# Kernel tuning notes

Measured on AMD Instinct MI355X. Metric: run time of the kernel, lower is better.

## Reference

```python
import jax, jax.numpy as jnp
import numpy as np
import math

B = 128        # batch (= bipartite matching N)
L = 16         # detector layers (MAX_LAYER)
E = 768        # n_embd
D = E // 2     # RFF target_dim
H = 12         # n_head
HD = E // H    # head_size
NL = 6         # n_layer
SEQ = 12       # tokens after concats: 3+3 -> 6 -> +currentLayer -> 12
MAX_LAYER = L
LN_EPS = 1e-3  # keras LayerNormalization default


def setup_inputs() -> dict:
    key = jax.random.key(0)
    ks = jax.random.split(key, 8)
    inp = {}
    inp["X"] = jax.random.normal(ks[0], (B, L, 3), dtype=jnp.float32) * 50.0
    inp["targets"] = jax.random.normal(ks[1], (B, L, 3), dtype=jnp.float32)
    # RandomFourierFeatures params (random per-call in original; fixed here):
    # x: xmin=-160,xmax=160,n=9*1024 ; y: n=12*512 ; dE: xmin=0,xmax=230,n=2300
    specs = [(-160.0, 160.0, 9 * 1024), (-160.0, 160.0, 12 * 512), (0.0, 230.0, 2300)]
    om, ph = [], []
    for i, (xmin, xmax, n) in enumerate(specs):
        k1, k2 = jax.random.split(jax.random.fold_in(ks[2], i))
        omin = 2.0 * math.pi / (xmax - xmin)
        lo, hi = math.log(omin / n), math.log(omin)
        om.append(jnp.exp(jax.random.uniform(k1, (D,), minval=lo, maxval=hi)))
        ph.append(jax.random.uniform(k2, (D,)))  # B ~ U(0,1)*scale, scale=1
    inp["omegas"] = jnp.stack(om).astype(jnp.float32)  # (3, D)
    inp["phases"] = jnp.stack(ph).astype(jnp.float32)  # (3, D)
    # np.random.permutation per layer-step, fixed here
    inp["perms"] = jnp.stack(
        [jax.random.permutation(jax.random.fold_in(ks[3], i), B) for i in range(L - 1)]
    ).astype(jnp.int32)  # (L-1, B)
    # transformer weights (stacked over layers)
    kk = jax.random.split(ks[4], 16)
    s = 0.02
    inp["Wq"] = jax.random.normal(kk[0], (NL, E, H, HD)) * s
    inp["bq"] = jnp.zeros((NL, H, HD))
    inp["Wk"] = jax.random.normal(kk[1], (NL, E, H, HD)) * s
    inp["bk"] = jnp.zeros((NL, H, HD))
    inp["Wv"] = jax.random.normal(kk[2], (NL, E, H, HD)) * s
    inp["bv"] = jnp.zeros((NL, H, HD))
    inp["Wo"] = jax.random.normal(kk[3], (NL, H, HD, E)) * s
    inp["bo"] = jnp.zeros((NL, E))
    inp["ln1g"] = jnp.ones((NL, E)); inp["ln1b"] = jnp.zeros((NL, E))
    inp["ln2g"] = jnp.ones((NL, E)); inp["ln2b"] = jnp.zeros((NL, E))
    inp["W1"] = jax.random.normal(kk[4], (NL, E, 4 * E)) * s
    inp["b1f"] = jnp.zeros((NL, 4 * E))
    inp["W2"] = jax.random.normal(kk[5], (NL, 4 * E, E)) * s
    inp["b2f"] = jnp.zeros((NL, E))
    inp["lnfg"] = jnp.ones((E,)); inp["lnfb"] = jnp.zeros((E,))
    inp["Wout"] = jax.random.normal(kk[6], (SEQ * E, 3)) * s
    inp["bout"] = jnp.zeros((3,))
    return inp


def _ln(x, g, b):
    mu = jnp.mean(x, -1, keepdims=True)
    v = jnp.var(x, -1, keepdims=True)
    return (x - mu) * jax.lax.rsqrt(v + LN_EPS) * g + b


def _greedy_match(cost):
    """Greedy bipartite matching: sort all NxN costs ascending, assign first-come.
    Returns row_to_col_match_vec (N,) int32."""
    N = cost.shape[0]
    order = jnp.argsort(cost.reshape(-1))

    def step(carry, k):
        row, col = carry
        i = k // N
        j = k % N
        ok = (row[i] == -1) & (col[j] == -1)
        row = row.at[i].set(jnp.where(ok, j, row[i]))
        col = col.at[j].set(jnp.where(ok, i, col[j]))
        return (row, col), None

    init = (jnp.full((N,), -1, jnp.int32), jnp.full((N,), -1, jnp.int32))
    (row, _), _ = jax.lax.scan(step, init, order)
    return row


def _forward(X, targets, omegas, phases, perms, Wq, bq, Wk, bk, Wv, bv, Wo, bo,
             ln1g, ln1b, ln2g, ln2b, W1, b1f, W2, b2f, lnfg, lnfb, Wout, bout):
    # RFF: (B,L,3) -> (B,L,3,D)
    XS = jnp.cos(X[..., None] * omegas[None, None, :, :] + phases[None, None, :, :])
    losses = []
    scale = 1.0 / math.sqrt(HD)
    for lidx in range(1, L):
        xc = XS[:, -lidx]        # (B,3,D)
        xp = XS[:, -lidx - 1]    # (B,3,D)
        x = jnp.concatenate([xc, xp], axis=2)            # (B,3,E)
        y = targets[:, -lidx + 1]                        # (B,3)
        y_prev = jnp.broadcast_to(y[:, :, None], (B, 3, E))
        x = jnp.concatenate([x, y_prev], axis=1)         # (B,6,E)
        cur = jnp.full_like(x, float(MAX_LAYER - lidx))
        x = jnp.concatenate([x, cur], axis=1)            # (B,12,E)
        x = x[perms[lidx - 1]]                           # batch permutation
        for l in range(NL):
            h = _ln(x, ln1g[l], ln1b[l])
            q = jnp.einsum('bse,ehd->bshd', h, Wq[l]) + bq[l]
            k = jnp.einsum('bse,ehd->bshd', h, Wk[l]) + bk[l]
            v = jnp.einsum('bse,ehd->bshd', h, Wv[l]) + bv[l]
            att = jax.nn.softmax(jnp.einsum('bqhd,bkhd->bhqk', q, k) * scale, axis=-1)
            o = jnp.einsum('bhqk,bkhd->bqhd', att, v)
            x = x + (jnp.einsum('bqhd,hde->bqe', o, Wo[l]) + bo[l])
            h = _ln(x, ln2g[l], ln2b[l])
            x = x + (jnp.maximum(h @ W1[l] + b1f[l], 0.0) @ W2[l] + b2f[l])
        x = _ln(x, lnfg, lnfb).reshape(B, SEQ * E)
        logits = x @ Wout + bout                         # (B,3)
        tgt = targets[:, -lidx]                          # (B,3)
        cost = jnp.sqrt(jnp.sum((logits[:, None, :] - tgt[None, :, :]) ** 2, axis=-1) + 1e-12)
        m = _greedy_match(jax.lax.stop_gradient(cost))
        lm = logits[m]                                   # gather per original
        losses.append(jnp.mean((lm - tgt) ** 2))
    return jnp.mean(jnp.stack(losses))


def reference(X, targets, omegas, phases, perms, Wq, bq, Wk, bk, Wv, bv, Wo, bo,
              ln1g, ln1b, ln2g, ln2b, W1, b1f, W2, b2f, lnfg, lnfb, Wout, bout):
    return _forward(X, targets, omegas, phases, perms, Wq, bq, Wk, bk, Wv, bv, Wo, bo,
                    ln1g, ln1b, ln2g, ln2b, W1, b1f, W2, b2f, lnfg, lnfb, Wout, bout)
```

## Files before the change

kernel.cpp:

```cpp
#include <hip/hip_runtime.h>
#include <hip/hip_bf16.h>
#include <math.h>

#define B_   128
#define L_   16
#define E_   768
#define D_   384
#define H_   12
#define HD_  64
#define NL_  6
#define SEQ_ 12
#define LN_EPS 0.001f
#define WLS   7077888
#define BQS   2304

typedef __attribute__((ext_vector_type(8))) short bf16x8;
typedef __attribute__((ext_vector_type(4))) float f32x4;
typedef unsigned long long u64;

#define GLOAD_LDS16(g, l) \
    __builtin_amdgcn_global_load_lds((__attribute__((address_space(1))) const void*)(g), \
                                     (__attribute__((address_space(3))) void*)(l), 16, 0, 0)

__global__ __launch_bounds__(256) void k_x0(const float* __restrict__ X,
                                            const float* __restrict__ targets,
                                            const int* __restrict__ perms,
                                            const float* __restrict__ om,
                                            const float* __restrict__ ph,
                                            float* __restrict__ x, int cb, int ntok) {
    int i = blockIdx.x * 256 + threadIdx.x;
    if (i >= ntok*E_) return;
    int e   = i % E_;
    int tok = i / E_;
    int s   = tok % SEQ_;
    int bi  = (tok / SEQ_) % B_;
    int c   = tok / (SEQ_*B_);
    int cl  = cb + c;
    int lidx = cl + 1;
    int pb  = perms[cl*B_ + bi];
    float val;
    if (s < 3) {
        int t  = (e < D_) ? (L_ - lidx) : (L_ - lidx - 1);
        int dd = (e < D_) ? e : (e - D_);
        float xv = X[(pb*L_ + t)*3 + s];
        val = cosf(xv * om[s*D_ + dd] + ph[s*D_ + dd]);
    } else if (s < 6) {
        int t = (17 - lidx) & 15;
        val = targets[(pb*L_ + t)*3 + (s - 3)];
    } else {
        val = (float)(L_ - lidx);
    }
    x[i] = val;
}

__global__ __launch_bounds__(256) void k_ln(const float* __restrict__ x,
                                            const float* __restrict__ g,
                                            const float* __restrict__ b,
                                            __hip_bfloat16* __restrict__ h) {
    int gi = blockIdx.x * 256 + threadIdx.x;
    int tok = gi >> 6, lane = gi & 63;
    const float4* xr = (const float4*)(x + (size_t)tok * E_);
    float4 v0 = xr[lane], v1 = xr[lane + 64], v2 = xr[lane + 128];
    float s = v0.x+v0.y+v0.z+v0.w + v1.x+v1.y+v1.z+v1.w + v2.x+v2.y+v2.z+v2.w;
    #pragma unroll
    for (int o = 32; o > 0; o >>= 1) s += __shfl_xor(s, o, 64);
    float mu = s * (1.0f / E_);
    v0.x-=mu; v0.y-=mu; v0.z-=mu; v0.w-=mu;
    v1.x-=mu; v1.y-=mu; v1.z-=mu; v1.w-=mu;
    v2.x-=mu; v2.y-=mu; v2.z-=mu; v2.w-=mu;
    float q = v0.x*v0.x+v0.y*v0.y+v0.z*v0.z+v0.w*v0.w
            + v1.x*v1.x+v1.y*v1.y+v1.z*v1.z+v1.w*v1.w
            + v2.x*v2.x+v2.y*v2.y+v2.z*v2.z+v2.w*v2.w;
    #pragma unroll
    for (int o = 32; o > 0; o >>= 1) q += __shfl_xor(q, o, 64);
    float rstd = rsqrtf(q * (1.0f / E_) + LN_EPS);
    const float4* g4 = (const float4*)g;
    const float4* b4 = (const float4*)b;
    ushort4* h4 = (ushort4*)(h + (size_t)tok * E_);
    #pragma unroll
    for (int k = 0; k < 3; k++) {
        float4 v = (k == 0) ? v0 : (k == 1) ? v1 : v2;
        float4 gg = g4[lane + k*64], bb = b4[lane + k*64];
        ushort4 o;
        o.x = __bfloat16_as_ushort(__float2bfloat16(v.x * rstd * gg.x + bb.x));
        o.y = __bfloat16_as_ushort(__float2bfloat16(v.y * rstd * gg.y + bb.y));
        o.z = __bfloat16_as_ushort(__float2bfloat16(v.z * rstd * gg.z + bb.z));
        o.w = __bfloat16_as_ushort(__float2bfloat16(v.w * rstd * gg.w + bb.w));
        h4[lane + k*64] = o;
    }
}

__global__ __launch_bounds__(256) void k_cvt(const float* __restrict__ Wq,
                                             const float* __restrict__ Wk,
                                             const float* __restrict__ Wv,
                                             const float* __restrict__ Wo,
                                             const float* __restrict__ W1,
                                             const float* __restrict__ W2,
                                             const float* __restrict__ bq,
                                             const float* __restrict__ bk,
                                             const float* __restrict__ bv,
                                             __hip_bfloat16* __restrict__ wl0,
                                             float* __restrict__ bqkv0, int lbase) {
    int bid = blockIdx.x;
    int l   = lbase + bid / 6913;
    bid %= 6913;
    __hip_bfloat16* wl = wl0 + (size_t)(l - lbase) * WLS;
    float* bqkv = bqkv0 + (l - lbase) * BQS;
    int tid = threadIdx.x;
    if (bid == 6912) {
        for (int i = tid; i < 2304; i += 256) {
            float v = (i < 768) ? bq[l*768 + i] : (i < 1536) ? bk[l*768 + i - 768]
                                                             : bv[l*768 + i - 1536];
            bqkv[i] = v;
        }
        return;
    }
    const float* src; __hip_bfloat16* dst; int K, N, ti, tj;
    if (bid < 1728) {
        int part = bid / 576, idx = bid % 576;
        const float* srcs[3] = {Wq, Wk, Wv};
        src = srcs[part] + (size_t)l*768*768; dst = wl + (size_t)part*768*768;
        K = 768; N = 768; tj = idx % 24; ti = idx / 24;
    } else if (bid < 2304) {
        int idx = bid - 1728;
        src = Wo + (size_t)l*768*768; dst = wl + 1769472;
        K = 768; N = 768; tj = idx % 24; ti = idx / 24;
    } else if (bid < 4608) {
        int idx = bid - 2304;
        src = W1 + (size_t)l*768*3072; dst = wl + 2359296;
        K = 768; N = 3072; tj = idx % 96; ti = idx / 96;
    } else {
        int idx = bid - 4608;
        src = W2 + (size_t)l*3072*768; dst = wl + 4718592;
        K = 3072; N = 768; tj = idx % 24; ti = idx / 24;
    }
    __shared__ float tbuf[32][33];
    int tx = tid & 31, ty = tid >> 5;
    #pragma unroll
    for (int p = 0; p < 4; p++) {
        int k = ti*32 + ty + p*8, n = tj*32 + tx;
        tbuf[ty + p*8][tx] = src[(size_t)k*N + n];
    }
    __syncthreads();
    #pragma unroll
    for (int p = 0; p < 4; p++) {
        int n = tj*32 + ty + p*8, k = ti*32 + tx;
        dst[(size_t)n*K + k] = __float2bfloat16(tbuf[tx][ty + p*8]);
    }
}

template<int BN_>
__global__ __launch_bounds__(256) void k_gemm_t(const __hip_bfloat16* __restrict__ A,
                                                const __hip_bfloat16* __restrict__ Bt,
                                                const float* __restrict__ bias,
                                                void* __restrict__ Cp,
                                                int K, int ldb, int ldc, int flags) {
    constexpr int NF = BN_ / 32;
    __shared__ __align__(16) char smem[8192 + BN_*64];
    char* As = smem;
    char* Bs = smem + 8192;
    int tid = threadIdx.x;
    int lane = tid & 63;
    int w = tid >> 6;
    int wm = (w >> 1) * 64, wn = (w & 1) * (BN_/2);
    int m0 = blockIdx.y * 128, n0 = blockIdx.x * BN_;

    int u1 = tid, u2 = tid + 256;
    int r1 = u1 >> 2, kg1 = ((u1 & 3) ^ ((r1 >> 1) & 3)) * 8;
    int r2 = u2 >> 2, kg2 = ((u2 & 3) ^ ((r2 >> 1) & 3)) * 8;

    f32x4 acc[4][NF] = {};
    int fr = lane & 15, fkg = lane >> 4;

    for (int k0 = 0; k0 < K; k0 += 32) {
        GLOAD_LDS16(A  + (size_t)(m0 + r1) * K   + k0 + kg1, As + u1 * 16);
        GLOAD_LDS16(A  + (size_t)(m0 + r2) * K   + k0 + kg2, As + u2 * 16);
        GLOAD_LDS16(Bt + (size_t)(n0 + r1) * ldb + k0 + kg1, Bs + u1 * 16);
        if (BN_ == 128)
            GLOAD_LDS16(Bt + (size_t)(n0 + r2) * ldb + k0 + kg2, Bs + u2 * 16);
        __syncthreads();
        bf16x8 a[4], b[NF];
        #pragma unroll
        for (int i = 0; i < 4; i++) {
            int m = wm + i*16 + fr;
            a[i] = *(const bf16x8*)(As + m*64 + ((fkg ^ ((m >> 1) & 3)) * 16));
        }
        #pragma unroll
        for (int j = 0; j < NF; j++) {
            int n = wn + j*16 + fr;
            b[j] = *(const bf16x8*)(Bs + n*64 + ((fkg ^ ((n >> 1) & 3)) * 16));
        }
        #pragma unroll
        for (int i = 0; i < 4; i++)
            #pragma unroll
            for (int j = 0; j < NF; j++)
                acc[i][j] = __builtin_amdgcn_mfma_f32_16x16x32_bf16(a[i], b[j], acc[i][j], 0, 0, 0);
        __syncthreads();
    }

    int colL = lane & 15, rowg = (lane >> 4) * 4;
    #pragma unroll
    for (int i = 0; i < 4; i++) {
        #pragma unroll
        for (int j = 0; j < NF; j++) {
            int col = n0 + wn + j*16 + colL;
            float bv = bias ? bias[col] : 0.0f;
            #pragma unroll
            for (int r = 0; r < 4; r++) {
                int row = m0 + wm + i*16 + rowg + r;
                float v = acc[i][j][r] + bv;
                if (flags & 4) v = fmaxf(v, 0.0f);
                size_t off = (size_t)row * ldc + col;
                if (flags & 1)      ((__hip_bfloat16*)Cp)[off] = __float2bfloat16(v);
                else if (flags & 2) ((float*)Cp)[off] += v;
                else                ((float*)Cp)[off] = v;
            }
        }
    }
}

__global__ __launch_bounds__(256) void k_attn(const __hip_bfloat16* __restrict__ qkv,
                                              __hip_bfloat16* __restrict__ o) {
    __shared__ float qs[SEQ_][HD_], ks[SEQ_][HD_], vs[SEQ_][HD_];
    __shared__ float att[SEQ_][SEQ_];
    int blk = blockIdx.x;
    int hh  = blk % H_;
    int cbb = blk / H_;
    int t = threadIdx.x;
    if (t < 96) {
        int s = t >> 3, c = (t & 7) * 8;
        size_t base = (size_t)(cbb*SEQ_ + s) * 2304 + hh*64 + c;
        bf16x8 q8 = *(const bf16x8*)(qkv + base);
        bf16x8 k8 = *(const bf16x8*)(qkv + base + 768);
        bf16x8 v8 = *(const bf16x8*)(qkv + base + 1536);
        #pragma unroll
        for (int j = 0; j < 8; j++) {
            qs[s][c+j] = __uint_as_float((unsigned)(unsigned short)q8[j] << 16);
            ks[s][c+j] = __uint_as_float((unsigned)(unsigned short)k8[j] << 16);
            vs[s][c+j] = __uint_as_float((unsigned)(unsigned short)v8[j] << 16);
        }
    }
    __syncthreads();
    if (t < SEQ_*SEQ_) {
        int qi = t / SEQ_, kj = t % SEQ_;
        float s = 0.f;
        #pragma unroll
        for (int d = 0; d < HD_; d++) s += qs[qi][d] * ks[kj][d];
        att[qi][kj] = s * 0.125f;
    }
    __syncthreads();
    if (t < SEQ_) {
        float mx = -1e30f;
        #pragma unroll
        for (int j = 0; j < SEQ_; j++) mx = fmaxf(mx, att[t][j]);
        float e[SEQ_]; float sum = 0.f;
        #pragma unroll
        for (int j = 0; j < SEQ_; j++) { e[j] = expf(att[t][j] - mx); sum += e[j]; }
        float inv = 1.f / sum;
        #pragma unroll
        for (int j = 0; j < SEQ_; j++) att[t][j] = e[j] * inv;
    }
    __syncthreads();
    for (int i = t; i < SEQ_*HD_; i += 256) {
        int s = i / HD_, d = i % HD_;
        float acc = 0.f;
        #pragma unroll
        for (int j = 0; j < SEQ_; j++) acc += att[s][j] * vs[j][d];
        o[(size_t)(cbb*SEQ_ + s) * 768 + hh*64 + d] = __float2bfloat16(acc);
    }
}

__global__ __launch_bounds__(256) void k_logits(const __hip_bfloat16* __restrict__ hfin,
                                                const float* __restrict__ Wout,
                                                const float* __restrict__ bout,
                                                float* __restrict__ logits, int cb) {
    __shared__ float red[3][256];
    int blk = blockIdx.x;
    int t = threadIdx.x;
    const __hip_bfloat16* row = hfin + (size_t)blk * SEQ_ * E_;
    float a0 = 0.f, a1 = 0.f, a2 = 0.f;
    for (int e = t; e < SEQ_*E_; e += 256) {
        float x = __bfloat162float(row[e]);
        a0 += x * Wout[e*3 + 0]; a1 += x * Wout[e*3 + 1]; a2 += x * Wout[e*3 + 2];
    }
    red[0][t] = a0; red[1][t] = a1; red[2][t] = a2;
    __syncthreads();
    for (int o = 128; o > 0; o >>= 1) {
        if (t < o) { red[0][t] += red[0][t+o]; red[1][t] += red[1][t+o]; red[2][t] += red[2][t+o]; }
        __syncthreads();
    }
    if (t < 3) logits[((size_t)cb*B_ + blk)*3 + t] = red[t][0] + bout[t];
}

__global__ __launch_bounds__(64) void k_match(const float* __restrict__ logits,
                                              const float* __restrict__ targets,
                                              float* __restrict__ losses) {
    __shared__ float cst[128 * 129];
    __shared__ float tg[128][3];
    __shared__ int mrow[128];
    int cl = blockIdx.x, lane = threadIdx.x;
    int lidx = cl + 1;
    for (int j = lane; j < 128; j += 64) {
        const float* tp = &targets[((size_t)j*L_ + (L_ - lidx)) * 3];
        tg[j][0] = tp[0]; tg[j][1] = tp[1]; tg[j][2] = tp[2];
    }
    __syncthreads();
    u64 kc[2];
    #pragma unroll
    for (int hh = 0; hh < 2; hh++) {
        int r = lane + hh*64;
        const float* lg = &logits[(cl*B_ + r) * 3];
        float l0 = lg[0], l1 = lg[1], l2 = lg[2];
        u64 best = ~0ull;
        for (int c = 0; c < 128; c++) {
            float d0 = l0 - tg[c][0], d1 = l1 - tg[c][1], d2 = l2 - tg[c][2];
            float cc = sqrtf(d0*d0 + d1*d1 + d2*d2 + 1e-12f);
            cst[r*129 + c] = cc;
            u64 key = ((u64)__float_as_uint(cc) << 14) | (unsigned)(r*128 + c);
            best = key < best ? key : best;
        }
        kc[hh] = best;
    }
    __syncthreads();
    u64 dead0 = 0, dead1 = 0;
    int done = 0;
    for (int trip = 0; trip < 16640 && done < 128; trip++) {
        u64 b = kc[0] < kc[1] ? kc[0] : kc[1];
        #pragma unroll
        for (int o = 32; o > 0; o >>= 1) {
            u64 x = __shfl_xor(b, o, 64);
            b = x < b ? x : b;
        }
        unsigned e  = (unsigned)b & 0x3fffu;
        unsigned wi = e >> 7, wj = e & 127;
        bool isDead = (((wj < 64) ? (dead0 >> wj) : (dead1 >> (wj - 64))) & 1ull) != 0;
        if (!isDead) {
            if ((wi & 63u) == (unsigned)lane) {
                mrow[wi] = (int)wj;
                kc[wi >> 6] = ~0ull;
            }
            if (wj < 64) dead0 |= 1ull << wj; else dead1 |= 1ull << (wj - 64);
            done++;
        } else {
            float c0 = cst[wi*129 + lane];
            float c1 = cst[wi*129 + lane + 64];
            bool d0b = ((dead0 >> lane) & 1ull) != 0;
            bool d1b = ((dead1 >> lane) & 1ull) != 0;
            u64 k0 = d0b ? ~0ull : (((u64)__float_as_uint(c0) << 14) | (unsigned)(wi*128 + lane));
            u64 k1 = d1b ? ~0ull : (((u64)__float_as_uint(c1) << 14) | (unsigned)(wi*128 + lane + 64));
            u64 nb = k0 < k1 ? k0 : k1;
            #pragma unroll
            for (int o = 32; o > 0; o >>= 1) {
                u64 x = __shfl_xor(nb, o, 64);
                nb = x < nb ? x : nb;
            }
            if ((wi & 63u) == (unsigned)lane) kc[wi >> 6] = nb;
        }
    }
    __syncthreads();
    float a = 0.f;
    #pragma unroll
    for (int hh = 0; hh < 2; hh++) {
        int r = lane + hh*64;
        const float* lg = &logits[(cl*B_ + mrow[r]) * 3];
        float d0 = lg[0]-tg[r][0], d1 = lg[1]-tg[r][1], d2 = lg[2]-tg[r][2];
        a += d0*d0 + d1*d1 + d2*d2;
    }
    #pragma unroll
    for (int o = 32; o > 0; o >>= 1) a += __shfl_xor(a, o, 64);
    if (lane == 0) losses[cl] = a * (1.0f / (B_*3));
}

__global__ void k_final(const float* __restrict__ losses, float* __restrict__ out) {
    float s = 0.f;
    for (int i = 0; i < 15; i++) s += losses[i];
    out[0] = s * (1.0f / 15.0f);
}

extern "C" void kernel_launch(void* const* d_in, const int* in_sizes, int n_in,
                              void* d_out, int out_size, void* d_ws, size_t ws_size,
                              hipStream_t stream) {
    (void)in_sizes; (void)n_in; (void)out_size;
    const float* X       = (const float*)d_in[0];
    const float* targets = (const float*)d_in[1];
    const float* omegas  = (const float*)d_in[2];
    const float* phases  = (const float*)d_in[3];
    const int*   perms   = (const int*)d_in[4];
    const float* Wq  = (const float*)d_in[5];
    const float* bq  = (const float*)d_in[6];
    const float* Wk  = (const float*)d_in[7];
    const float* bk  = (const float*)d_in[8];
    const float* Wv  = (const float*)d_in[9];
    const float* bv  = (const float*)d_in[10];
    const float* Wo  = (const float*)d_in[11];
    const float* bo  = (const float*)d_in[12];
    const float* ln1g = (const float*)d_in[13];
    const float* ln1b = (const float*)d_in[14];
    const float* ln2g = (const float*)d_in[15];
    const float* ln2b = (const float*)d_in[16];
    const float* W1  = (const float*)d_in[17];
    const float* b1f = (const float*)d_in[18];
    const float* W2  = (const float*)d_in[19];
    const float* b2f = (const float*)d_in[20];
    const float* lnfg = (const float*)d_in[21];
    const float* lnfb = (const float*)d_in[22];
    const float* Wout = (const float*)d_in[23];
    const float* bout = (const float*)d_in[24];

    int CL; bool hoist;
    if (ws_size >= 263000000ull)      { CL = 15; hoist = false; }
    else if (ws_size >= 169000000ull) { CL = 5;  hoist = true;  }
    else                              { CL = 5;  hoist = false; }
    int M = CL * B_ * SEQ_;
    bool perLayerCvt = (CL == 15) || !hoist;

    char* wsb = (char*)d_ws;
    size_t off = 0;
    auto alloc = [&](size_t bytes) {
        char* p = wsb + off;
        off += (bytes + 255) & ~(size_t)255;
        return p;
    };
    float*          x      = (float*)alloc((size_t)M*E_*4);
    __hip_bfloat16* h      = (__hip_bfloat16*)alloc((size_t)M*E_*2);
    __hip_bfloat16* qkvh   = (__hip_bfloat16*)alloc((size_t)M*3072*2);
    __hip_bfloat16* wl     = (__hip_bfloat16*)alloc((hoist ? 6 : 1) * (size_t)WLS*2);
    float*          bqkv   = (float*)alloc((hoist ? 6 : 1) * (size_t)BQS*4);
    float*          logits = (float*)alloc(23040);
    float*          losses = (float*)alloc(64);

    if (hoist)
        k_cvt<<<6*6913, 256, 0, stream>>>(Wq, Wk, Wv, Wo, W1, W2, bq, bk, bv, wl, bqkv, 0);

    dim3 gQKV(2304/128, M/128);
    dim3 gF1 (3072/128, M/128);
    dim3 gN64(768/64,   M/128);
    dim3 gLN (M/4);

    for (int cb = 0; cb < 15; cb += CL) {
        k_x0<<<(M*E_)/256, 256, 0, stream>>>(X, targets, perms, omegas, phases, x, cb, M);
        for (int l = 0; l < NL_; l++) {
            __hip_bfloat16* wlp = hoist ? wl + (size_t)l*WLS : wl;
            float*          bqp = hoist ? bqkv + l*BQS : bqkv;
            if (perLayerCvt)
                k_cvt<<<6913, 256, 0, stream>>>(Wq, Wk, Wv, Wo, W1, W2, bq, bk, bv, wlp, bqp, l);
            k_ln<<<gLN, 256, 0, stream>>>(x, ln1g + l*E_, ln1b + l*E_, h);
            k_gemm_t<128><<<gQKV, 256, 0, stream>>>(h, wlp, bqp, qkvh, 768, 768, 2304, 1);
            k_attn<<<CL*B_*H_, 256, 0, stream>>>(qkvh, h);
            k_gemm_t<64><<<gN64, 256, 0, stream>>>(h, wlp + 1769472, bo + l*E_, x,
                                                   768, 768, 768, 2);
            k_ln<<<gLN, 256, 0, stream>>>(x, ln2g + l*E_, ln2b + l*E_, h);
            k_gemm_t<128><<<gF1, 256, 0, stream>>>(h, wlp + 2359296, b1f + l*3072, qkvh,
                                                   768, 768, 3072, 1|4);
            k_gemm_t<64><<<gN64, 256, 0, stream>>>(qkvh, wlp + 4718592, b2f + l*E_, x,
                                                   3072, 3072, 768, 2);
        }
        k_ln<<<gLN, 256, 0, stream>>>(x, lnfg, lnfb, h);
        k_logits<<<CL*B_, 256, 0, stream>>>(h, Wout, bout, logits, cb);
    }
    k_match<<<15, 64, 0, stream>>>(logits, targets, losses);
    k_final<<<1, 1, 0, stream>>>(losses, (float*)d_out);
}
```

Before: 5.075 ms.

## Replace GEMM with 256x256 double-buffered, 8-wave pipelined MFMA kernel

Replaces the 128xBN single-buffered GEMM with a 256x256-tile kernel of 512 threads that uses 128KB of LDS with double buffering and BK=64. Prefetching of the next k-tile is interleaved with MFMA phases, using explicit barriers and s_setprio. The aim is to raise arithmetic intensity and hide global-load latency. In exchange, it launches far fewer blocks (e.g. 3 column blocks for N=768), which can leave CUs idle when M is small. The very large LDS footprint also limits occupancy.

```diff
diff --git a/kernel.cpp b/kernel.cpp
--- a/kernel.cpp
+++ b/kernel.cpp
@@ -149,65 +149,142 @@
     }
 }
 
-template<int BN_>
-__global__ __launch_bounds__(256) void k_gemm_t(const __hip_bfloat16* __restrict__ A,
-                                                const __hip_bfloat16* __restrict__ Bt,
-                                                const float* __restrict__ bias,
-                                                void* __restrict__ Cp,
-                                                int K, int ldb, int ldc, int flags) {
-    constexpr int NF = BN_ / 32;
-    __shared__ __align__(16) char smem[8192 + BN_*64];
-    char* As = smem;
-    char* Bs = smem + 8192;
-    int tid = threadIdx.x;
-    int lane = tid & 63;
-    int w = tid >> 6;
-    int wm = (w >> 1) * 64, wn = (w & 1) * (BN_/2);
-    int m0 = blockIdx.y * 128, n0 = blockIdx.x * BN_;
-
-    int u1 = tid, u2 = tid + 256;
-    int r1 = u1 >> 2, kg1 = ((u1 & 3) ^ ((r1 >> 1) & 3)) * 8;
-    int r2 = u2 >> 2, kg2 = ((u2 & 3) ^ ((r2 >> 1) & 3)) * 8;
-
-    f32x4 acc[4][NF] = {};
-    int fr = lane & 15, fkg = lane >> 4;
-
-    for (int k0 = 0; k0 < K; k0 += 32) {
-        GLOAD_LDS16(A  + (size_t)(m0 + r1) * K   + k0 + kg1, As + u1 * 16);
-        GLOAD_LDS16(A  + (size_t)(m0 + r2) * K   + k0 + kg2, As + u2 * 16);
-        GLOAD_LDS16(Bt + (size_t)(n0 + r1) * ldb + k0 + kg1, Bs + u1 * 16);
-        if (BN_ == 128)
-            GLOAD_LDS16(Bt + (size_t)(n0 + r2) * ldb + k0 + kg2, Bs + u2 * 16);
-        __syncthreads();
-        bf16x8 a[4], b[NF];
-        #pragma unroll
-        for (int i = 0; i < 4; i++) {
-            int m = wm + i*16 + fr;
-            a[i] = *(const bf16x8*)(As + m*64 + ((fkg ^ ((m >> 1) & 3)) * 16));
-        }
-        #pragma unroll
-        for (int j = 0; j < NF; j++) {
-            int n = wn + j*16 + fr;
-            b[j] = *(const bf16x8*)(Bs + n*64 + ((fkg ^ ((n >> 1) & 3)) * 16));
-        }
+#define MFMA_BF16(a, b, c) __builtin_amdgcn_mfma_f32_16x16x32_bf16(a, b, c, 0, 0, 0)
+
+__global__ __launch_bounds__(512) void k_gemm256(const __hip_bfloat16* __restrict__ A,
+                                                 const __hip_bfloat16* __restrict__ Bt,
+                                                 const float* __restrict__ bias,
+                                                 void* __restrict__ Cp,
+                                                 int K, int ldb, int ldc, int flags) {
+    __shared__ __align__(16) char smem[131072];
+    const int tid  = threadIdx.x;
+    const int lane = tid & 63;
+    const int wid  = tid >> 6;
+    const int wr   = wid >> 2;
+    const int wc   = wid & 3;
+    const int m0   = blockIdx.y * 256;
+    const int n0   = blockIdx.x * 256;
+    const int fr   = lane & 15, fkg = lane >> 4, sx = fr & 7;
+    const int NT   = K >> 6;
+
+    const int srow = tid >> 3;
+    const int skc  = 8 * ((tid & 7) ^ ((tid >> 3) & 7));
+
+    const int aoff0 = (wr*128 + fr)*128 + (((0*4 + fkg) ^ sx) << 4);
+    const int aoff1 = (wr*128 + fr)*128 + (((1*4 + fkg) ^ sx) << 4);
+    const int boff0 = 32768 + (wc*64 + fr)*128 + (((0*4 + fkg) ^ sx) << 4);
+    const int boff1 = 32768 + (wc*64 + fr)*128 + (((1*4 + fkg) ^ sx) << 4);
+
+    f32x4 acc[8][4] = {};
+
+    auto stage = [&](int kt, int buf, int h) {
+        const __hip_bfloat16* mat = (h & 2) ? Bt : A;
+        const int ld   = (h & 2) ? ldb : K;
+        const int row0 = ((h & 2) ? n0 : m0) + (h & 1)*128;
+        char* d = smem + buf*65536 + ((h & 2) ? 32768 : 0) + (h & 1)*16384;
+        const int kk = kt*64 + skc;
+        GLOAD_LDS16(mat + (size_t)(row0 + srow)      * ld + kk, d + tid*16);
+        GLOAD_LDS16(mat + (size_t)(row0 + 64 + srow) * ld + kk, d + 8192 + tid*16);
+    };
+    auto ldA = [&](int buf, int i, int ks) -> bf16x8 {
+        return *(const bf16x8*)(smem + buf*65536 + i*2048 + (ks ? aoff1 : aoff0));
+    };
+    auto ldB = [&](int buf, int j, int ks) -> bf16x8 {
+        return *(const bf16x8*)(smem + buf*65536 + j*2048 + (ks ? boff1 : boff0));
+    };
+
+    stage(0, 0, 0); stage(0, 0, 1); stage(0, 0, 2); stage(0, 0, 3);
+    asm volatile("s_waitcnt vmcnt(0)" ::: "memory");
+    __syncthreads();
+
+    bf16x8 a[4][2], blo[2][2], bhi[2][2];
+
+    for (int kt = 0; kt < NT; ++kt) {
+        const int cur = kt & 1, nxt = cur ^ 1;
+        const bool pf = (kt + 1 < NT);
+
+        #pragma unroll
+        for (int i = 0; i < 4; i++) { a[i][0] = ldA(cur, i, 0); a[i][1] = ldA(cur, i, 1); }
+        #pragma unroll
+        for (int j = 0; j < 2; j++) { blo[j][0] = ldB(cur, j, 0); blo[j][1] = ldB(cur, j, 1); }
+        if (pf) { stage(kt+1, nxt, 0); stage(kt+1, nxt, 1); }
+        __builtin_amdgcn_sched_barrier(0);
+        __builtin_amdgcn_s_barrier();
+        asm volatile("s_waitcnt lgkmcnt(0)" ::: "memory");
+        __builtin_amdgcn_sched_barrier(0);
+        __builtin_amdgcn_s_setprio(1);
         #pragma unroll
         for (int i = 0; i < 4; i++)
             #pragma unroll
-            for (int j = 0; j < NF; j++)
-                acc[i][j] = __builtin_amdgcn_mfma_f32_16x16x32_bf16(a[i], b[j], acc[i][j], 0, 0, 0);
+            for (int j = 0; j < 2; j++) {
+                acc[i][j] = MFMA_BF16(a[i][0], blo[j][0], acc[i][j]);
+                acc[i][j] = MFMA_BF16(a[i][1], blo[j][1], acc[i][j]);
+            }
+        __builtin_amdgcn_s_setprio(0);
+        __builtin_amdgcn_sched_barrier(0);
+        __builtin_amdgcn_s_barrier();
+
+        #pragma unroll
+        for (int j = 0; j < 2; j++) { bhi[j][0] = ldB(cur, j+2, 0); bhi[j][1] = ldB(cur, j+2, 1); }
+        if (pf) { stage(kt+1, nxt, 2); stage(kt+1, nxt, 3); }
+        __builtin_amdgcn_sched_barrier(0);
+        __builtin_amdgcn_s_barrier();
+        asm volatile("s_waitcnt lgkmcnt(0)" ::: "memory");
+        __builtin_amdgcn_sched_barrier(0);
+        __builtin_amdgcn_s_setprio(1);
+        #pragma unroll
+        for (int i = 0; i < 4; i++)
+            #pragma unroll
+            for (int j = 0; j < 2; j++) {
+                acc[i][j+2] = MFMA_BF16(a[i][0], bhi[j][0], acc[i][j+2]);
+                acc[i][j+2] = MFMA_BF16(a[i][1], bhi[j][1], acc[i][j+2]);
+            }
+        __builtin_amdgcn_s_setprio(0);
+        __builtin_amdgcn_sched_barrier(0);
+        __builtin_amdgcn_s_barrier();
+
+        #pragma unroll
+        for (int i = 0; i < 4; i++) { a[i][0] = ldA(cur, i+4, 0); a[i][1] = ldA(cur, i+4, 1); }
+        __builtin_amdgcn_sched_barrier(0);
+        __builtin_amdgcn_s_barrier();
+        asm volatile("s_waitcnt lgkmcnt(0)" ::: "memory");
+        __builtin_amdgcn_sched_barrier(0);
+        __builtin_amdgcn_s_setprio(1);
+        #pragma unroll
+        for (int i = 0; i < 4; i++)
+            #pragma unroll
+            for (int j = 0; j < 2; j++) {
+                acc[i+4][j+2] = MFMA_BF16(a[i][0], bhi[j][0], acc[i+4][j+2]);
+                acc[i+4][j+2] = MFMA_BF16(a[i][1], bhi[j][1], acc[i+4][j+2]);
+            }
+        __builtin_amdgcn_s_setprio(0);
+        __builtin_amdgcn_sched_barrier(0);
+        __builtin_amdgcn_s_barrier();
+
+        __builtin_amdgcn_s_setprio(1);
+        #pragma unroll
+        for (int i = 0; i < 4; i++)
+            #pragma unroll
+            for (int j = 0; j < 2; j++) {
+                acc[i+4][j] = MFMA_BF16(a[i][0], blo[j][0], acc[i+4][j]);
+                acc[i+4][j] = MFMA_BF16(a[i][1], blo[j][1], acc[i+4][j]);
+            }
+        __builtin_amdgcn_s_setprio(0);
+        __builtin_amdgcn_sched_barrier(0);
+        asm volatile("s_waitcnt vmcnt(0)" ::: "memory");
         __syncthreads();
     }
 
-    int colL = lane & 15, rowg = (lane >> 4) * 4;
-    #pragma unroll
-    for (int i = 0; i < 4; i++) {
-        #pragma unroll
-        for (int j = 0; j < NF; j++) {
-            int col = n0 + wn + j*16 + colL;
+    const int colL = lane & 15, rowg = (lane >> 4) * 4;
+    #pragma unroll
+    for (int i = 0; i < 8; i++) {
+        #pragma unroll
+        for (int j = 0; j < 4; j++) {
+            int col = n0 + wc*64 + j*16 + colL;
             float bv = bias ? bias[col] : 0.0f;
             #pragma unroll
             for (int r = 0; r < 4; r++) {
-                int row = m0 + wm + i*16 + rowg + r;
+                int row = m0 + wr*128 + i*16 + rowg + r;
                 float v = acc[i][j][r] + bv;
                 if (flags & 4) v = fmaxf(v, 0.0f);
                 size_t off = (size_t)row * ldc + col;
@@ -432,9 +509,9 @@
     if (hoist)
         k_cvt<<<6*6913, 256, 0, stream>>>(Wq, Wk, Wv, Wo, W1, W2, bq, bk, bv, wl, bqkv, 0);
 
-    dim3 gQKV(2304/128, M/128);
-    dim3 gF1 (3072/128, M/128);
-    dim3 gN64(768/64,   M/128);
+    dim3 gQKV(2304/256, M/256);
+    dim3 gF1 (3072/256, M/256);
+    dim3 gN  (768/256,  M/256);
     dim3 gLN (M/4);
 
     for (int cb = 0; cb < 15; cb += CL) {
@@ -445,15 +522,15 @@
             if (perLayerCvt)
                 k_cvt<<<6913, 256, 0, stream>>>(Wq, Wk, Wv, Wo, W1, W2, bq, bk, bv, wlp, bqp, l);
             k_ln<<<gLN, 256, 0, stream>>>(x, ln1g + l*E_, ln1b + l*E_, h);
-            k_gemm_t<128><<<gQKV, 256, 0, stream>>>(h, wlp, bqp, qkvh, 768, 768, 2304, 1);
+            k_gemm256<<<gQKV, 512, 0, stream>>>(h, wlp, bqp, qkvh, 768, 768, 2304, 1);
             k_attn<<<CL*B_*H_, 256, 0, stream>>>(qkvh, h);
-            k_gemm_t<64><<<gN64, 256, 0, stream>>>(h, wlp + 1769472, bo + l*E_, x,
-                                                   768, 768, 768, 2);
+            k_gemm256<<<gN, 512, 0, stream>>>(h, wlp + 1769472, bo + l*E_, x,
+                                              768, 768, 768, 2);
             k_ln<<<gLN, 256, 0, stream>>>(x, ln2g + l*E_, ln2b + l*E_, h);
-            k_gemm_t<128><<<gF1, 256, 0, stream>>>(h, wlp + 2359296, b1f + l*3072, qkvh,
-                                                   768, 768, 3072, 1|4);
-            k_gemm_t<64><<<gN64, 256, 0, stream>>>(qkvh, wlp + 4718592, b2f + l*E_, x,
-                                                   3072, 3072, 768, 2);
+            k_gemm256<<<gF1, 512, 0, stream>>>(h, wlp + 2359296, b1f + l*3072, qkvh,
+                                               768, 768, 3072, 1|4);
+            k_gemm256<<<gN, 512, 0, stream>>>(qkvh, wlp + 4718592, b2f + l*E_, x,
+                                              3072, 3072, 768, 2);
         }
         k_ln<<<gLN, 256, 0, stream>>>(x, lnfg, lnfb, h);
         k_logits<<<CL*B_, 256, 0, stream>>>(h, Wout, bout, logits, cb);
```

Result: slower. 5.211 ms (+2.7%).
